# Optimization experiments

Measured on AMD Instinct MI355X. Metric: run time of the kernel, lower is better.

## Reference

```python
import jax, jax.numpy as jnp
import numpy as np

D_MODEL = 1024
NHEAD = 16
HEAD_DIM = D_MODEL // NHEAD
ROPE_BASE = 10000.0


def _rope_freq(T, head_dim):
    half = head_dim // 2
    pos = jnp.arange(T, dtype=jnp.float32)
    idx = jnp.arange(half, dtype=jnp.float32)
    freq_div = ROPE_BASE ** (2.0 * idx / head_dim)
    return pos[:, None] / freq_div[None, :]  # [T, half]


def _rope_rotate(x, cos, sin):
    # x: [B, H, T, d]; cos/sin: [T, d//2]
    half = x.shape[-1] // 2
    xl, xr = x[..., :half], x[..., half:]
    c = cos[None, None]
    s = sin[None, None]
    return jnp.concatenate([xl * c - xr * s, xl * s + xr * c], axis=-1)


def setup_inputs() -> dict:
    key = jax.random.key(0)
    ks = jax.random.split(key, 12)
    B, T = 2, 2048
    sd = 1.0 / np.sqrt(D_MODEL)
    inp = {
        "query": jax.random.normal(ks[0], (B, T, D_MODEL), jnp.float32),
        "key": jax.random.normal(ks[1], (B, T, D_MODEL), jnp.float32),
        "value": jax.random.normal(ks[2], (B, T, D_MODEL), jnp.float32),
        "frac": jax.random.uniform(ks[3], (B, T), jnp.float32),
        # Linear weights stored [in, out] (torch W.T)
        "Wq": jax.random.normal(ks[4], (D_MODEL, D_MODEL), jnp.float32) * sd,
        "Wk": jax.random.normal(ks[5], (D_MODEL, D_MODEL), jnp.float32) * sd,
        "Wv": jax.random.normal(ks[6], (D_MODEL, D_MODEL), jnp.float32) * sd,
        "Wo": jax.random.normal(ks[7], (D_MODEL, D_MODEL), jnp.float32) * sd,
        "bq": jnp.zeros((D_MODEL,), jnp.float32),
        "bk": jnp.zeros((D_MODEL,), jnp.float32),
        "bv": jnp.zeros((D_MODEL,), jnp.float32),
        "bo": jnp.zeros((D_MODEL,), jnp.float32),
        "alpha_pos": jax.random.normal(ks[8], (NHEAD,), jnp.float32) * 0.1,
        "alpha_neg": jax.random.normal(ks[9], (NHEAD,), jnp.float32) * 0.1,
    }
    return inp


def reference(query, key, value, frac, Wq, Wk, Wv, Wo, bq, bk, bv, bo, alpha_pos, alpha_neg):
    B, T, dm = query.shape
    H, hd = NHEAD, HEAD_DIM
    scale = hd ** -0.5

    def split_heads(x):  # [B,T,dm] -> [B,H,T,hd]
        return x.reshape(B, T, H, hd).transpose(0, 2, 1, 3)

    Q = split_heads(query @ Wq + bq)
    K = split_heads(key @ Wk + bk)
    V = split_heads(value @ Wv + bv)

    freq = _rope_freq(T, hd)
    cos, sin = jnp.cos(freq), jnp.sin(freq)
    Q = _rope_rotate(Q, cos, sin)
    K = _rope_rotate(K, cos, sin)

    scores = jnp.einsum("bhqd,bhkd->bhqk", Q, K) * scale  # [B,H,T,T]

    # data-dependent stoichiometric bias
    D = frac[:, None, :] - frac[:, :, None]  # [B,T,T], D[b,i,j] = frac_j - frac_i
    D_pos = jax.nn.relu(D)
    D_neg = -jax.nn.relu(-D)
    bias = (alpha_pos[None, :, None, None] * D_pos[:, None] +
            alpha_neg[None, :, None, None] * D_neg[:, None])  # [B,H,T,T]
    scores = scores + bias

    probs = jax.nn.softmax(scores, axis=-1)
    out = jnp.einsum("bhqk,bhkd->bhqd", probs, V)  # [B,H,T,hd]
    out = out.transpose(0, 2, 1, 3).reshape(B, T, dm)
    return out @ Wo + bo
```

## Files before the change

### kernel.cpp

```cpp
#include <hip/hip_runtime.h>


typedef unsigned short u16;
typedef __bf16 bf8v __attribute__((ext_vector_type(8)));
typedef __bf16 bf4v __attribute__((ext_vector_type(4)));
typedef float f32x4 __attribute__((ext_vector_type(4)));

#define D_MODEL 1024
#define T_SEQ   2048
#define NHEAD   16
#define HDIM    64
#define BATCH   2
#define M_TOT   (BATCH * T_SEQ)
#define LOG2E   1.4426950408889634f

__device__ __forceinline__ void gl2lds16(const u16* g, u16* l) {
  __builtin_amdgcn_global_load_lds(
      (__attribute__((address_space(1))) void*)g,
      (__attribute__((address_space(3))) void*)l, 16, 0, 0);
}

__global__ __launch_bounds__(256) void k_prep(
    const float* __restrict__ q, const float* __restrict__ k,
    const float* __restrict__ v, const float* __restrict__ Wq,
    const float* __restrict__ Wk, const float* __restrict__ Wv,
    const float* __restrict__ Wo, u16* __restrict__ Xb, u16* __restrict__ WtB,
    float* __restrict__ ct, float* __restrict__ st) {
  __shared__ float tile[64 * 65];
  int bx = blockIdx.x, tid = threadIdx.x;
  if (bx < 6144) {
    int z = bx >> 11, xb = bx & 2047;
    const float* src = (z == 0) ? q : (z == 1) ? k : v;
    u16* dst = Xb + (size_t)z * (M_TOT * D_MODEL);
    int idx = (xb * 256 + tid) * 8;
    float4 a = *(const float4*)(src + idx);
    float4 b = *(const float4*)(src + idx + 4);
    bf8v o;
    o[0] = (__bf16)a.x; o[1] = (__bf16)a.y; o[2] = (__bf16)a.z; o[3] = (__bf16)a.w;
    o[4] = (__bf16)b.x; o[5] = (__bf16)b.y; o[6] = (__bf16)b.z; o[7] = (__bf16)b.w;
    *(bf8v*)(dst + idx) = o;
  } else if (bx < 7168) {
    int idx2 = bx - 6144;
    int z = idx2 >> 8, rem = idx2 & 255;
    int k0 = (rem >> 4) * 64, n0 = (rem & 15) * 64;
    const float* W = (z == 0) ? Wq : (z == 1) ? Wk : (z == 2) ? Wv : Wo;
    u16* Wt = WtB + (size_t)z * (D_MODEL * D_MODEL);
#pragma unroll
    for (int i = 0; i < 16; i++) {
      int idx = tid + i * 256;
      int r = idx >> 6, c = idx & 63;
      tile[c * 65 + r] = W[(size_t)(k0 + r) * D_MODEL + n0 + c];
    }
    __syncthreads();
#pragma unroll
    for (int i = 0; i < 16; i++) {
      int idx = tid + i * 256;
      int r = idx >> 6, c = idx & 63;
      ((__bf16*)Wt)[(size_t)(n0 + r) * D_MODEL + k0 + c] = (__bf16)tile[r * 65 + c];
    }
  } else {
    int idx = (bx - 7168) * 256 + tid;
    int t = idx >> 5, d = idx & 31;
    float ang = (float)t * powf(10000.0f, -(float)d * (1.0f / 32.0f));
    ct[idx] = cosf(ang);
    st[idx] = sinf(ang);
  }
}

__device__ __forceinline__ void gemm_core_128(const u16* __restrict__ A,
                                              const u16* __restrict__ Bt,
                                              u16* sA, u16* sB,
                                              f32x4 (&acc)[4][4],
                                              int m0, int n0) {
  const int K = D_MODEL;
  int tid = threadIdx.x;
  int lane = tid & 63, wave = tid >> 6;
  int l15 = lane & 15, quad = lane >> 4;
  int wm = (wave >> 1) * 64, wn = (wave & 1) * 64;
  int r0 = tid >> 2, pcol0 = (tid & 3) * 8;
  int r1 = 64 + r0;
  const u16* A0 = A + (size_t)(m0 + r0) * K + pcol0;
  const u16* A1 = A + (size_t)(m0 + r1) * K + pcol0;
  const u16* B0 = Bt + (size_t)(n0 + r0) * K + pcol0;
  const u16* B1 = Bt + (size_t)(n0 + r1) * K + pcol0;
  u16* dA0 = sA + wave * 512;
  u16* dA1 = sA + 2048 + wave * 512;
  u16* dB0 = sB + wave * 512;
  u16* dB1 = sB + 2048 + wave * 512;
  for (int k0 = 0; k0 < K; k0 += 64) {
    __syncthreads();
    gl2lds16(A0 + k0, dA0);
    gl2lds16(A1 + k0, dA1);
    gl2lds16(A0 + k0 + 32, dA0 + 4096);
    gl2lds16(A1 + k0 + 32, dA1 + 4096);
    gl2lds16(B0 + k0, dB0);
    gl2lds16(B0 + k0 + 32, dB0 + 4096);
    gl2lds16(B1 + k0, dB1);
    gl2lds16(B1 + k0 + 32, dB1 + 4096);
    __syncthreads();
#pragma unroll
    for (int kh = 0; kh < 2; kh++) {
      bf8v af[4], bf[4];
#pragma unroll
      for (int i = 0; i < 4; i++)
        af[i] = *(const bf8v*)(sA + kh * 4096 + (wm + i * 16 + l15) * 32 + quad * 8);
#pragma unroll
      for (int i = 0; i < 4; i++)
        bf[i] = *(const bf8v*)(sB + kh * 4096 + (wn + i * 16 + l15) * 32 + quad * 8);
#pragma unroll
      for (int mi = 0; mi < 4; mi++)
#pragma unroll
        for (int ni = 0; ni < 4; ni++)
          acc[mi][ni] = __builtin_amdgcn_mfma_f32_16x16x32_bf16(
              af[mi], bf[ni], acc[mi][ni], 0, 0, 0);
    }
  }
}

__global__ __launch_bounds__(256) void k_gemm_qkv(
    const u16* __restrict__ Xb, const u16* __restrict__ WtB,
    const float* __restrict__ bq, const float* __restrict__ bk,
    const float* __restrict__ bv, const float* __restrict__ ctab,
    const float* __restrict__ stab, u16* __restrict__ OutB,
    u16* __restrict__ Vb) {
  __shared__ __align__(16) u16 sA[128 * 64];
  __shared__ __align__(16) u16 sB[128 * 64];
  int z = blockIdx.z;
  const u16* A = Xb + (size_t)z * (M_TOT * D_MODEL);
  const u16* Bt = WtB + (size_t)z * (D_MODEL * D_MODEL);
  const float* bias = (z == 0) ? bq : (z == 1) ? bk : bv;
  u16* Out = OutB + (size_t)z * (M_TOT * D_MODEL);
  int m0 = blockIdx.y * 128, n0 = blockIdx.x * 128;
  f32x4 acc[4][4] = {};
  gemm_core_128(A, Bt, sA, sB, acc, m0, n0);

  int tid = threadIdx.x, lane = tid & 63, wave = tid >> 6;
  int l15 = lane & 15, quad = lane >> 4;
  int wm = (wave >> 1) * 64, wn = (wave & 1) * 64;
  float bvv[4];
#pragma unroll
  for (int ni = 0; ni < 4; ni++) bvv[ni] = bias[n0 + wn + ni * 16 + l15];

  if (z < 2) {
    float qs = (z == 0) ? 0.125f * LOG2E : 1.0f;
#pragma unroll
    for (int mi = 0; mi < 4; mi++) {
#pragma unroll
      for (int r = 0; r < 4; r++) {
        int m = m0 + wm + mi * 16 + quad * 4 + r;
        size_t ro = (size_t)m * D_MODEL + n0 + wn;
        int tl = m & (T_SEQ - 1);
#pragma unroll
        for (int ni = 0; ni < 2; ni++) {
          int d = ni * 16 + l15;
          float c = ctab[tl * 32 + d], s = stab[tl * 32 + d];
          float xl = acc[mi][ni][r] + bvv[ni];
          float xr = acc[mi][ni + 2][r] + bvv[ni + 2];
          ((__bf16*)Out)[ro + d] = (__bf16)((xl * c - xr * s) * qs);
          ((__bf16*)Out)[ro + d + 32] = (__bf16)((xl * s + xr * c) * qs);
        }
      }
    }
  } else {
    int hh = (n0 + wn) >> 6;
    int mbase = m0 + wm;
    int bb = mbase >> 11;
    int tbase = mbase & (T_SEQ - 1);
    u16* Vw = Vb + (size_t)(bb * NHEAD + hh) * HDIM * T_SEQ;
#pragma unroll
    for (int mi = 0; mi < 4; mi++)
#pragma unroll
      for (int r = 0; r < 4; r++) {
        int t = tbase + mi * 16 + quad * 4 + r;
#pragma unroll
        for (int ni = 0; ni < 4; ni++) {
          int d = ni * 16 + l15;
          ((__bf16*)Vw)[(size_t)d * T_SEQ + t] = (__bf16)(acc[mi][ni][r] + bvv[ni]);
        }
      }
  }
}

__global__ __launch_bounds__(256) void k_gemm_out(
    const u16* __restrict__ ctx, const u16* __restrict__ Wot,
    const float* __restrict__ bo, float* __restrict__ Cout) {
  __shared__ __align__(16) u16 sA[64 * 64];
  __shared__ __align__(16) u16 sB[64 * 64];
  const int K = D_MODEL;
  int m0 = blockIdx.y * 64, n0 = blockIdx.x * 64;
  int tid = threadIdx.x, lane = tid & 63, wave = tid >> 6;
  int l15 = lane & 15, quad = lane >> 4;
  int wm = (wave >> 1) * 32, wn = (wave & 1) * 32;
  int r0 = tid >> 2, pcol0 = (tid & 3) * 8;
  const u16* A0 = ctx + (size_t)(m0 + r0) * K + pcol0;
  const u16* B0 = Wot + (size_t)(n0 + r0) * K + pcol0;
  u16* dA = sA + wave * 512;
  u16* dB = sB + wave * 512;
  f32x4 acc[2][2] = {};
  for (int k0 = 0; k0 < K; k0 += 64) {
    __syncthreads();
    gl2lds16(A0 + k0, dA);
    gl2lds16(A0 + k0 + 32, dA + 2048);
    gl2lds16(B0 + k0, dB);
    gl2lds16(B0 + k0 + 32, dB + 2048);
    __syncthreads();
#pragma unroll
    for (int kh = 0; kh < 2; kh++) {
      bf8v af[2], bf[2];
#pragma unroll
      for (int i = 0; i < 2; i++)
        af[i] = *(const bf8v*)(sA + kh * 2048 + (wm + i * 16 + l15) * 32 + quad * 8);
#pragma unroll
      for (int i = 0; i < 2; i++)
        bf[i] = *(const bf8v*)(sB + kh * 2048 + (wn + i * 16 + l15) * 32 + quad * 8);
#pragma unroll
      for (int mi = 0; mi < 2; mi++)
#pragma unroll
        for (int ni = 0; ni < 2; ni++)
          acc[mi][ni] = __builtin_amdgcn_mfma_f32_16x16x32_bf16(
              af[mi], bf[ni], acc[mi][ni], 0, 0, 0);
    }
  }
  float bvv[2];
#pragma unroll
  for (int ni = 0; ni < 2; ni++) bvv[ni] = bo[n0 + wn + ni * 16 + l15];
#pragma unroll
  for (int mi = 0; mi < 2; mi++)
#pragma unroll
    for (int r = 0; r < 4; r++) {
      size_t ro = (size_t)(m0 + wm + mi * 16 + quad * 4 + r) * D_MODEL + n0 + wn;
#pragma unroll
      for (int ni = 0; ni < 2; ni++)
        Cout[ro + ni * 16 + l15] = acc[mi][ni][r] + bvv[ni];
    }
}

__global__ __launch_bounds__(256) void k_attn(
    const u16* __restrict__ Qr, const u16* __restrict__ Kr,
    const u16* __restrict__ Vb, const float* __restrict__ frac,
    const float* __restrict__ alpha_pos, const float* __restrict__ alpha_neg,
    u16* __restrict__ ctx) {
  __shared__ __align__(16) u16 kT[2][64 * 64];
  __shared__ __align__(16) u16 vT[2][64 * 64];
  __shared__ __align__(16) u16 pT[4][2][16 * 72];
  int bh = blockIdx.y, b = bh >> 4, h = bh & 15;
  int q0 = blockIdx.x * 128;
  int tid = threadIdx.x, wave = tid >> 6, lane = tid & 63;
  int l15 = lane & 15, quad = lane >> 4;

  const u16* Kh = Kr + (size_t)b * T_SEQ * D_MODEL + h * HDIM;
  const u16* Vh = Vb + (size_t)bh * HDIM * T_SEQ;
  const float* fb = frac + b * T_SEQ;

  bf8v qf[2][2];
  float fq[2];
#pragma unroll
  for (int g = 0; g < 2; g++) {
    int qrow = q0 + wave * 32 + g * 16 + l15;
    const u16* qbase =
        Qr + (size_t)(b * T_SEQ + qrow) * D_MODEL + h * HDIM + quad * 8;
    qf[g][0] = *(const bf8v*)qbase;
    qf[g][1] = *(const bf8v*)(qbase + 32);
    fq[g] = fb[qrow];
  }
  float ap = alpha_pos[h] * LOG2E, an = alpha_neg[h] * LOG2E;
  bf8v onesv;
#pragma unroll
  for (int j = 0; j < 8; j++) onesv[j] = (__bf16)1.0f;
  f32x4 o[2][4] = {};
  f32x4 o_l[2] = {};
  u16* pw = &pT[wave][0][0];

  int x0 = (quad ^ (l15 & 7)) * 8;
  int kidx[4], vidx[4];
#pragma unroll
  for (int nt = 0; nt < 4; nt++) kidx[nt] = ((nt * 16 + l15) << 6) + x0;
#pragma unroll
  for (int dt = 0; dt < 4; dt++) vidx[dt] = ((dt * 16 + l15) << 6) + x0;
  int pidx = l15 * 72 + quad * 8;

  int p0 = tid, p1 = 256 + tid;
  int kr0 = p0 >> 3, gc0 = (p0 & 7) ^ (kr0 & 7);
  int kr1 = p1 >> 3, gc1 = (p1 & 7) ^ (kr1 & 7);
  const u16* kg0 = Kh + (size_t)kr0 * D_MODEL + gc0 * 8;
  const u16* kg1 = Kh + (size_t)kr1 * D_MODEL + gc1 * 8;
  const u16* vg0 = Vh + (size_t)kr0 * T_SEQ + gc0 * 8;
  const u16* vg1 = Vh + (size_t)kr1 * T_SEQ + gc1 * 8;
  int woff = wave * 512;

  auto stage = [&](int buf, int kbase) {
    gl2lds16(kg0 + (size_t)kbase * D_MODEL, kT[buf] + woff);
    gl2lds16(kg1 + (size_t)kbase * D_MODEL, kT[buf] + 2048 + woff);
    gl2lds16(vg0 + kbase, vT[buf] + woff);
    gl2lds16(vg1 + kbase, vT[buf] + 2048 + woff);
  };

  stage(0, 0);
  __syncthreads();

  for (int kt = 0; kt < T_SEQ / 64; kt++) {
    int kbase = kt * 64;
    int buf = kt & 1;
    if (kt + 1 < T_SEQ / 64) stage(buf ^ 1, kbase + 64);
    const u16* kb = kT[buf];
    const u16* vb = vT[buf];

    bf8v kf0[4], kf1[4];
#pragma unroll
    for (int nt = 0; nt < 4; nt++) {
      kf0[nt] = *(const bf8v*)(kb + kidx[nt]);
      kf1[nt] = *(const bf8v*)(kb + (kidx[nt] ^ 32));
    }
    bf8v vf[2][4];
#pragma unroll
    for (int dt = 0; dt < 4; dt++) {
      vf[0][dt] = *(const bf8v*)(vb + vidx[dt]);
      vf[1][dt] = *(const bf8v*)(vb + (vidx[dt] ^ 32));
    }
    f32x4 fk4[4];
#pragma unroll
    for (int nt = 0; nt < 4; nt++)
      fk4[nt] = *(const f32x4*)(fb + kbase + nt * 16 + quad * 4);

#pragma unroll
    for (int g = 0; g < 2; g++) {
      float fqg = fq[g];
      u16* pwg = pw + g * (16 * 72);
#pragma unroll
      for (int nt = 0; nt < 4; nt++) {
        f32x4 s = {};
        s = __builtin_amdgcn_mfma_f32_16x16x32_bf16(kf0[nt], qf[g][0], s, 0, 0, 0);
        s = __builtin_amdgcn_mfma_f32_16x16x32_bf16(kf1[nt], qf[g][1], s, 0, 0, 0);
        bf4v pk;
#pragma unroll
        for (int r = 0; r < 4; r++) {
          float dd = fk4[nt][r] - fqg;
          float sel = (dd >= 0.0f) ? ap : an;
          pk[r] = (__bf16)__builtin_amdgcn_exp2f(fmaf(dd, sel, s[r]));
        }
        *(bf4v*)(pwg + l15 * 72 + nt * 16 + quad * 4) = pk;
      }
      asm volatile("s_waitcnt lgkmcnt(0)" ::: "memory");
#pragma unroll
      for (int kc = 0; kc < 2; kc++) {
        bf8v pf = *(const bf8v*)(pwg + pidx + kc * 32);
        o_l[g] = __builtin_amdgcn_mfma_f32_16x16x32_bf16(pf, onesv, o_l[g], 0, 0, 0);
#pragma unroll
        for (int dt = 0; dt < 4; dt++)
          o[g][dt] = __builtin_amdgcn_mfma_f32_16x16x32_bf16(pf, vf[kc][dt],
                                                             o[g][dt], 0, 0, 0);
      }
    }
    __syncthreads();
  }

#pragma unroll
  for (int g = 0; g < 2; g++) {
#pragma unroll
    for (int r = 0; r < 4; r++) {
      float linv = 1.0f / o_l[g][r];
      int qg = q0 + wave * 32 + g * 16 + quad * 4 + r;
      __bf16* orow = (__bf16*)(ctx + (size_t)(b * T_SEQ + qg) * D_MODEL + h * HDIM);
#pragma unroll
      for (int dt = 0; dt < 4; dt++)
        orow[dt * 16 + l15] = (__bf16)(o[g][dt][r] * linv);
    }
  }
}

extern "C" void kernel_launch(void* const* d_in, const int* in_sizes, int n_in,
                              void* d_out, int out_size, void* d_ws,
                              size_t ws_size, hipStream_t stream) {
  const float* q = (const float*)d_in[0];
  const float* k = (const float*)d_in[1];
  const float* v = (const float*)d_in[2];
  const float* frac = (const float*)d_in[3];
  const float* Wq = (const float*)d_in[4];
  const float* Wk = (const float*)d_in[5];
  const float* Wv = (const float*)d_in[6];
  const float* Wo = (const float*)d_in[7];
  const float* bq = (const float*)d_in[8];
  const float* bk = (const float*)d_in[9];
  const float* bv = (const float*)d_in[10];
  const float* bo = (const float*)d_in[11];
  const float* alpha_pos = (const float*)d_in[12];
  const float* alpha_neg = (const float*)d_in[13];

  char* ws = (char*)d_ws;
  u16* Xb = (u16*)(ws + 0);
  u16* Wt = (u16*)(ws + 25165824);
  u16* Qr = (u16*)(ws + 33554432);
  u16* Kr = (u16*)(ws + 41943040);
  u16* Vtmp = (u16*)(ws + 50331648);
  u16* Vb = (u16*)(ws + 58720256);
  float* ctab = (float*)(ws + 67108864);
  float* stab = (float*)(ws + 67371008);
  u16* ctx = Vtmp;
  u16* QKVout = Qr;

  k_prep<<<dim3(7424), 256, 0, stream>>>(q, k, v, Wq, Wk, Wv, Wo, Xb, Wt, ctab,
                                         stab);
  k_gemm_qkv<<<dim3(8, 32, 3), 256, 0, stream>>>(Xb, Wt, bq, bk, bv, ctab, stab,
                                                 QKVout, Vb);
  k_attn<<<dim3(16, 32), 256, 0, stream>>>(Qr, Kr, Vb, frac, alpha_pos,
                                           alpha_neg, ctx);
  k_gemm_out<<<dim3(16, 64), 256, 0, stream>>>(ctx, Wt + 3 * 1048576, bo,
                                               (float*)d_out);
}
```

Measured before the change: 256.7 us.

## Fuse fp32-to-bf16 activation conversion into QKV GEMM A-tile loading

Removes the separate pass in the prep kernel that converted the q/k/v activations to bf16 in a workspace buffer. The QKV GEMM now reads fp32 activations directly into registers one k-tile ahead, converts them to bf16, and stores them into a padded LDS tile (row stride 72). This drops a full write and re-read of 24 MB of bf16 data. In exchange the GEMM reads twice as many A bytes per tile, goes through registers instead of the direct global-to-LDS path, and uses more registers. Attention index precomputation is also moved inline into the loop.

```diff
diff --git a/kernel.cpp b/kernel.cpp
--- a/kernel.cpp
+++ b/kernel.cpp
@@ -21,27 +21,13 @@
 }
 
 __global__ __launch_bounds__(256) void k_prep(
-    const float* __restrict__ q, const float* __restrict__ k,
-    const float* __restrict__ v, const float* __restrict__ Wq,
-    const float* __restrict__ Wk, const float* __restrict__ Wv,
-    const float* __restrict__ Wo, u16* __restrict__ Xb, u16* __restrict__ WtB,
-    float* __restrict__ ct, float* __restrict__ st) {
+    const float* __restrict__ Wq, const float* __restrict__ Wk,
+    const float* __restrict__ Wv, const float* __restrict__ Wo,
+    u16* __restrict__ WtB, float* __restrict__ ct, float* __restrict__ st) {
   __shared__ float tile[64 * 65];
   int bx = blockIdx.x, tid = threadIdx.x;
-  if (bx < 6144) {
-    int z = bx >> 11, xb = bx & 2047;
-    const float* src = (z == 0) ? q : (z == 1) ? k : v;
-    u16* dst = Xb + (size_t)z * (M_TOT * D_MODEL);
-    int idx = (xb * 256 + tid) * 8;
-    float4 a = *(const float4*)(src + idx);
-    float4 b = *(const float4*)(src + idx + 4);
-    bf8v o;
-    o[0] = (__bf16)a.x; o[1] = (__bf16)a.y; o[2] = (__bf16)a.z; o[3] = (__bf16)a.w;
-    o[4] = (__bf16)b.x; o[5] = (__bf16)b.y; o[6] = (__bf16)b.z; o[7] = (__bf16)b.w;
-    *(bf8v*)(dst + idx) = o;
-  } else if (bx < 7168) {
-    int idx2 = bx - 6144;
-    int z = idx2 >> 8, rem = idx2 & 255;
+  if (bx < 1024) {
+    int z = bx >> 8, rem = bx & 255;
     int k0 = (rem >> 4) * 64, n0 = (rem & 15) * 64;
     const float* W = (z == 0) ? Wq : (z == 1) ? Wk : (z == 2) ? Wv : Wo;
     u16* Wt = WtB + (size_t)z * (D_MODEL * D_MODEL);
@@ -59,7 +45,7 @@
       ((__bf16*)Wt)[(size_t)(n0 + r) * D_MODEL + k0 + c] = (__bf16)tile[r * 65 + c];
     }
   } else {
-    int idx = (bx - 7168) * 256 + tid;
+    int idx = (bx - 1024) * 256 + tid;
     int t = idx >> 5, d = idx & 31;
     float ang = (float)t * powf(10000.0f, -(float)d * (1.0f / 32.0f));
     ct[idx] = cosf(ang);
@@ -67,43 +53,74 @@
   }
 }
 
-__device__ __forceinline__ void gemm_core_128(const u16* __restrict__ A,
-                                              const u16* __restrict__ Bt,
-                                              u16* sA, u16* sB,
-                                              f32x4 (&acc)[4][4],
-                                              int m0, int n0) {
+__global__ __launch_bounds__(256) void k_gemm_qkv(
+    const float* __restrict__ qx, const float* __restrict__ kx,
+    const float* __restrict__ vx, const u16* __restrict__ WtB,
+    const float* __restrict__ bq, const float* __restrict__ bk,
+    const float* __restrict__ bv, const float* __restrict__ ctab,
+    const float* __restrict__ stab, u16* __restrict__ OutB,
+    u16* __restrict__ Vb) {
+  __shared__ __align__(16) u16 sA[128 * 72];
+  __shared__ __align__(16) u16 sB[128 * 64];
   const int K = D_MODEL;
-  int tid = threadIdx.x;
-  int lane = tid & 63, wave = tid >> 6;
+  int z = blockIdx.z;
+  const float* Xf = (z == 0) ? qx : (z == 1) ? kx : vx;
+  const u16* Bt = WtB + (size_t)z * (D_MODEL * D_MODEL);
+  const float* bias = (z == 0) ? bq : (z == 1) ? bk : bv;
+  u16* Out = OutB + (size_t)z * (M_TOT * D_MODEL);
+  int m0 = blockIdx.y * 128, n0 = blockIdx.x * 128;
+
+  int tid = threadIdx.x, lane = tid & 63, wave = tid >> 6;
   int l15 = lane & 15, quad = lane >> 4;
   int wm = (wave >> 1) * 64, wn = (wave & 1) * 64;
-  int r0 = tid >> 2, pcol0 = (tid & 3) * 8;
-  int r1 = 64 + r0;
-  const u16* A0 = A + (size_t)(m0 + r0) * K + pcol0;
-  const u16* A1 = A + (size_t)(m0 + r1) * K + pcol0;
+
+  int r0 = tid >> 2, q4 = tid & 3;
+  const float* Ag0 = Xf + (size_t)(m0 + r0) * K + q4 * 16;
+  const float* Ag1 = Ag0 + (size_t)64 * K;
+  u16* wA0 = sA + r0 * 72 + q4 * 16;
+  u16* wA1 = wA0 + 64 * 72;
+
+  int pcol0 = (tid & 3) * 8;
   const u16* B0 = Bt + (size_t)(n0 + r0) * K + pcol0;
-  const u16* B1 = Bt + (size_t)(n0 + r1) * K + pcol0;
-  u16* dA0 = sA + wave * 512;
-  u16* dA1 = sA + 2048 + wave * 512;
+  const u16* B1 = B0 + (size_t)64 * K;
   u16* dB0 = sB + wave * 512;
   u16* dB1 = sB + 2048 + wave * 512;
+
+  float4 va0[4], va1[4];
+  auto loadA = [&](int k0) {
+#pragma unroll
+    for (int c = 0; c < 4; c++) {
+      va0[c] = *(const float4*)(Ag0 + k0 + c * 4);
+      va1[c] = *(const float4*)(Ag1 + k0 + c * 4);
+    }
+  };
+  auto cvst = [&](u16* dst, const float4& a, const float4& b) {
+    bf8v t;
+    t[0] = (__bf16)a.x; t[1] = (__bf16)a.y; t[2] = (__bf16)a.z; t[3] = (__bf16)a.w;
+    t[4] = (__bf16)b.x; t[5] = (__bf16)b.y; t[6] = (__bf16)b.z; t[7] = (__bf16)b.w;
+    *(bf8v*)dst = t;
+  };
+
+  f32x4 acc[4][4] = {};
+  loadA(0);
   for (int k0 = 0; k0 < K; k0 += 64) {
     __syncthreads();
-    gl2lds16(A0 + k0, dA0);
-    gl2lds16(A1 + k0, dA1);
-    gl2lds16(A0 + k0 + 32, dA0 + 4096);
-    gl2lds16(A1 + k0 + 32, dA1 + 4096);
+    cvst(wA0, va0[0], va0[1]);
+    cvst(wA0 + 8, va0[2], va0[3]);
+    cvst(wA1, va1[0], va1[1]);
+    cvst(wA1 + 8, va1[2], va1[3]);
     gl2lds16(B0 + k0, dB0);
     gl2lds16(B0 + k0 + 32, dB0 + 4096);
     gl2lds16(B1 + k0, dB1);
     gl2lds16(B1 + k0 + 32, dB1 + 4096);
     __syncthreads();
+    if (k0 + 64 < K) loadA(k0 + 64);
 #pragma unroll
     for (int kh = 0; kh < 2; kh++) {
       bf8v af[4], bf[4];
 #pragma unroll
       for (int i = 0; i < 4; i++)
-        af[i] = *(const bf8v*)(sA + kh * 4096 + (wm + i * 16 + l15) * 32 + quad * 8);
+        af[i] = *(const bf8v*)(sA + (wm + i * 16 + l15) * 72 + kh * 32 + quad * 8);
 #pragma unroll
       for (int i = 0; i < 4; i++)
         bf[i] = *(const bf8v*)(sB + kh * 4096 + (wn + i * 16 + l15) * 32 + quad * 8);
@@ -115,28 +132,7 @@
               af[mi], bf[ni], acc[mi][ni], 0, 0, 0);
     }
   }
-}
-
-__global__ __launch_bounds__(256) void k_gemm_qkv(
-    const u16* __restrict__ Xb, const u16* __restrict__ WtB,
-    const float* __restrict__ bq, const float* __restrict__ bk,
-    const float* __restrict__ bv, const float* __restrict__ ctab,
-    const float* __restrict__ stab, u16* __restrict__ OutB,
-    u16* __restrict__ Vb) {
-  __shared__ __align__(16) u16 sA[128 * 64];
-  __shared__ __align__(16) u16 sB[128 * 64];
-  int z = blockIdx.z;
-  const u16* A = Xb + (size_t)z * (M_TOT * D_MODEL);
-  const u16* Bt = WtB + (size_t)z * (D_MODEL * D_MODEL);
-  const float* bias = (z == 0) ? bq : (z == 1) ? bk : bv;
-  u16* Out = OutB + (size_t)z * (M_TOT * D_MODEL);
-  int m0 = blockIdx.y * 128, n0 = blockIdx.x * 128;
-  f32x4 acc[4][4] = {};
-  gemm_core_128(A, Bt, sA, sB, acc, m0, n0);
-
-  int tid = threadIdx.x, lane = tid & 63, wave = tid >> 6;
-  int l15 = lane & 15, quad = lane >> 4;
-  int wm = (wave >> 1) * 64, wn = (wave & 1) * 64;
+
   float bvv[4];
 #pragma unroll
   for (int ni = 0; ni < 4; ni++) bvv[ni] = bias[n0 + wn + ni * 16 + l15];
@@ -271,14 +267,6 @@
   f32x4 o_l[2] = {};
   u16* pw = &pT[wave][0][0];
 
-  int x0 = (quad ^ (l15 & 7)) * 8;
-  int kidx[4], vidx[4];
-#pragma unroll
-  for (int nt = 0; nt < 4; nt++) kidx[nt] = ((nt * 16 + l15) << 6) + x0;
-#pragma unroll
-  for (int dt = 0; dt < 4; dt++) vidx[dt] = ((dt * 16 + l15) << 6) + x0;
-  int pidx = l15 * 72 + quad * 8;
-
   int p0 = tid, p1 = 256 + tid;
   int kr0 = p0 >> 3, gc0 = (p0 & 7) ^ (kr0 & 7);
   int kr1 = p1 >> 3, gc1 = (p1 & 7) ^ (kr1 & 7);
@@ -302,20 +290,21 @@
     int kbase = kt * 64;
     int buf = kt & 1;
     if (kt + 1 < T_SEQ / 64) stage(buf ^ 1, kbase + 64);
-    const u16* kb = kT[buf];
-    const u16* vb = vT[buf];
 
     bf8v kf0[4], kf1[4];
+    int x0 = (quad ^ (l15 & 7)) * 8;
 #pragma unroll
     for (int nt = 0; nt < 4; nt++) {
-      kf0[nt] = *(const bf8v*)(kb + kidx[nt]);
-      kf1[nt] = *(const bf8v*)(kb + (kidx[nt] ^ 32));
+      const u16* rb = kT[buf] + ((nt * 16 + l15) << 6);
+      kf0[nt] = *(const bf8v*)(rb + x0);
+      kf1[nt] = *(const bf8v*)(rb + (x0 ^ 32));
     }
     bf8v vf[2][4];
 #pragma unroll
     for (int dt = 0; dt < 4; dt++) {
-      vf[0][dt] = *(const bf8v*)(vb + vidx[dt]);
-      vf[1][dt] = *(const bf8v*)(vb + (vidx[dt] ^ 32));
+      const u16* rb = vT[buf] + ((dt * 16 + l15) << 6);
+      vf[0][dt] = *(const bf8v*)(rb + x0);
+      vf[1][dt] = *(const bf8v*)(rb + (x0 ^ 32));
     }
     f32x4 fk4[4];
 #pragma unroll
@@ -343,7 +332,7 @@
       asm volatile("s_waitcnt lgkmcnt(0)" ::: "memory");
 #pragma unroll
       for (int kc = 0; kc < 2; kc++) {
-        bf8v pf = *(const bf8v*)(pwg + pidx + kc * 32);
+        bf8v pf = *(const bf8v*)(pwg + l15 * 72 + kc * 32 + quad * 8);
         o_l[g] = __builtin_amdgcn_mfma_f32_16x16x32_bf16(pf, onesv, o_l[g], 0, 0, 0);
 #pragma unroll
         for (int dt = 0; dt < 4; dt++)
@@ -387,7 +376,6 @@
   const float* alpha_neg = (const float*)d_in[13];
 
   char* ws = (char*)d_ws;
-  u16* Xb = (u16*)(ws + 0);
   u16* Wt = (u16*)(ws + 25165824);
   u16* Qr = (u16*)(ws + 33554432);
   u16* Kr = (u16*)(ws + 41943040);
@@ -398,10 +386,9 @@
   u16* ctx = Vtmp;
   u16* QKVout = Qr;
 
-  k_prep<<<dim3(7424), 256, 0, stream>>>(q, k, v, Wq, Wk, Wv, Wo, Xb, Wt, ctab,
-                                         stab);
-  k_gemm_qkv<<<dim3(8, 32, 3), 256, 0, stream>>>(Xb, Wt, bq, bk, bv, ctab, stab,
-                                                 QKVout, Vb);
+  k_prep<<<dim3(1280), 256, 0, stream>>>(Wq, Wk, Wv, Wo, Wt, ctab, stab);
+  k_gemm_qkv<<<dim3(8, 32, 3), 256, 0, stream>>>(q, k, v, Wt, bq, bk, bv, ctab,
+                                                 stab, QKVout, Vb);
   k_attn<<<dim3(16, 32), 256, 0, stream>>>(Qr, Kr, Vb, frac, alpha_pos,
                                            alpha_neg, ctx);
   k_gemm_out<<<dim3(16, 64), 256, 0, stream>>>(ctx, Wt + 3 * 1048576, bo,
```

After: 268.0 us. +4.4%, slower.
